# Performance work log

Measured on AMD Instinct MI355X. Metric: run time of the kernel, lower is better.

The kernel has to match this reference:

```python
import jax, jax.numpy as jnp
import numpy as np

D = 1024
H = 16
FF = 4 * D


def layer_norm(x, g, b, eps=1e-5):
    mu = jnp.mean(x, axis=-1, keepdims=True)
    var = jnp.var(x, axis=-1, keepdims=True)
    return (x - mu) * jax.lax.rsqrt(var + eps) * g + b


def setup_inputs() -> dict:
    key = jax.random.key(0)
    ks = jax.random.split(key, 8)
    s = lambda fan_in: 1.0 / np.sqrt(fan_in)
    return {
        "x": jax.random.normal(ks[0], (2, 2048, D), dtype=jnp.float32),
        "ln1_g": jnp.ones((D,), jnp.float32),
        "ln1_b": jnp.zeros((D,), jnp.float32),
        "w_qkv": jax.random.uniform(ks[1], (D, 3 * D), jnp.float32, -s(D), s(D)),
        "b_qkv": jnp.zeros((3 * D,), jnp.float32),
        "w_out": jax.random.uniform(ks[2], (D, D), jnp.float32, -s(D), s(D)),
        "b_out": jnp.zeros((D,), jnp.float32),
        "ln2_g": jnp.ones((D,), jnp.float32),
        "ln2_b": jnp.zeros((D,), jnp.float32),
        "w_fc1": jax.random.uniform(ks[3], (D, FF), jnp.float32, -s(D), s(D)),
        "b_fc1": jnp.zeros((FF,), jnp.float32),
        "w_fc2": jax.random.uniform(ks[4], (FF, D), jnp.float32, -s(FF), s(FF)),
        "b_fc2": jnp.zeros((D,), jnp.float32),
    }


def reference(x, ln1_g, ln1_b, w_qkv, b_qkv, w_out, b_out,
              ln2_g, ln2_b, w_fc1, b_fc1, w_fc2, b_fc2):
    b, n, c = x.shape
    hd = c // H
    scale = hd ** -0.5

    # --- pre-norm MHA ---
    h = layer_norm(x, ln1_g, ln1_b)
    qkv = h @ w_qkv + b_qkv                      # [b,n,3c]
    qkv = qkv.reshape(b, n, 3, H, hd)
    q = jnp.transpose(qkv[:, :, 0], (0, 2, 1, 3))  # [b,H,n,hd]
    k = jnp.transpose(qkv[:, :, 1], (0, 2, 1, 3))
    v = jnp.transpose(qkv[:, :, 2], (0, 2, 1, 3))
    attn = jnp.einsum('bhqd,bhkd->bhqk', q, k) * scale
    attn = jax.nn.softmax(attn, axis=-1)
    o = jnp.einsum('bhqk,bhkd->bhqd', attn, v)   # [b,H,n,hd]
    o = jnp.transpose(o, (0, 2, 1, 3)).reshape(b, n, c)
    x = x + (o @ w_out + b_out)

    # --- pre-norm FFN ---
    h = layer_norm(x, ln2_g, ln2_b)
    h = jax.nn.gelu(h @ w_fc1 + b_fc1, approximate=False)
    x = x + (h @ w_fc2 + b_fc2)
    return x
```

## Files before the change

kernel.cpp:

```cpp
#include <hip/hip_runtime.h>
#include <stdint.h>
#include <math.h>

#define D_MODEL 1024
#define NHEAD   16
#define HDIM    64
#define FFDIM   4096
#define SEQ     2048
#define BATCH   2
#define NTOK    (BATCH*SEQ)
#define QKVN    (3*D_MODEL)

typedef __bf16 bf16;
typedef __attribute__((ext_vector_type(8))) __bf16 bf16x8;
typedef __attribute__((ext_vector_type(4))) __bf16 bf16x4;
typedef __attribute__((ext_vector_type(4))) float f32x4;

__device__ __forceinline__ void gld_lds16(const void* g, void* l) {
    __builtin_amdgcn_global_load_lds((__attribute__((address_space(1))) void*)g,
                                     (__attribute__((address_space(3))) void*)l,
                                     16, 0, 0);
}

__device__ __forceinline__ float fast_exp2(float x) {
#if __has_builtin(__builtin_amdgcn_exp2f)
    return __builtin_amdgcn_exp2f(x);
#else
    return __expf(x * 0.69314718056f);
#endif
}

#define GEMM_BAR() do {                                        \
    asm volatile("s_waitcnt lgkmcnt(0)" ::: "memory");         \
    __builtin_amdgcn_s_barrier();                              \
    asm volatile("" ::: "memory");                             \
} while (0)

__global__ __launch_bounds__(256)
void k_transpose_all(const float* __restrict__ w_qkv, const float* __restrict__ w_out,
                     const float* __restrict__ w_fc1, const float* __restrict__ w_fc2,
                     bf16* __restrict__ t_qkv, bf16* __restrict__ t_out,
                     bf16* __restrict__ t_fc1, bf16* __restrict__ t_fc2) {
    __shared__ float tile[32][33];
    int bid = blockIdx.x;
    const float* W; bf16* Wt; int K, N, ti;
    if (bid < 3072)       { W = w_qkv; Wt = t_qkv; K = 1024; N = 3072; ti = bid; }
    else if (bid < 4096)  { W = w_out; Wt = t_out; K = 1024; N = 1024; ti = bid - 3072; }
    else if (bid < 8192)  { W = w_fc1; Wt = t_fc1; K = 1024; N = 4096; ti = bid - 4096; }
    else                  { W = w_fc2; Wt = t_fc2; K = 4096; N = 1024; ti = bid - 8192; }
    int tn = N >> 5;
    int n0 = (ti % tn) * 32, k0 = (ti / tn) * 32;
    int tx = threadIdx.x, ty = threadIdx.y;
#pragma unroll
    for (int i = 0; i < 4; i++)
        tile[ty + i * 8][tx] = W[(size_t)(k0 + ty + i * 8) * N + n0 + tx];
    __syncthreads();
#pragma unroll
    for (int i = 0; i < 4; i++)
        Wt[(size_t)(n0 + ty + i * 8) * K + k0 + tx] = (bf16)tile[tx][ty + i * 8];
}

__global__ __launch_bounds__(256)
void k_vtrans(const bf16* __restrict__ qkv, bf16* __restrict__ vT) {
    __shared__ bf16 t[32][33];
    int tok0 = blockIdx.x * 32, f0 = blockIdx.y * 32;
    int tx = threadIdx.x, ty = threadIdx.y;
#pragma unroll
    for (int i = 0; i < 4; i++)
        t[ty + i * 8][tx] = qkv[(size_t)(tok0 + ty + i * 8) * QKVN + 2 * D_MODEL + f0 + tx];
    __syncthreads();
    int s = tx;
    int pp = (s < 16) ? ((s >> 2) * 8 + (s & 3))
                      : (((s - 16) >> 2) * 8 + ((s - 16) & 3) + 4);
#pragma unroll
    for (int i = 0; i < 4; i++)
        vT[(size_t)(f0 + ty + i * 8) * NTOK + tok0 + pp] = t[tx][ty + i * 8];
}

__global__ __launch_bounds__(256)
void k_layernorm(const float* __restrict__ x, const float* __restrict__ g,
                 const float* __restrict__ b, bf16* __restrict__ out) {
    int row = blockIdx.x;
    int tid = threadIdx.x;
    float4 v = ((const float4*)(x + (size_t)row * D_MODEL))[tid];
    float s  = v.x + v.y + v.z + v.w;
    float ss = v.x * v.x + v.y * v.y + v.z * v.z + v.w * v.w;
#pragma unroll
    for (int off = 32; off > 0; off >>= 1) {
        s  += __shfl_down(s, off, 64);
        ss += __shfl_down(ss, off, 64);
    }
    __shared__ float red[2][4];
    __shared__ float mv[2];
    int wave = tid >> 6, lane = tid & 63;
    if (lane == 0) { red[0][wave] = s; red[1][wave] = ss; }
    __syncthreads();
    if (tid == 0) {
        float S  = red[0][0] + red[0][1] + red[0][2] + red[0][3];
        float SS = red[1][0] + red[1][1] + red[1][2] + red[1][3];
        float mu = S * (1.0f / D_MODEL);
        float var = SS * (1.0f / D_MODEL) - mu * mu;
        mv[0] = mu;
        mv[1] = rsqrtf(var + 1e-5f);
    }
    __syncthreads();
    float mu = mv[0], rs = mv[1];
    float4 gv = ((const float4*)g)[tid];
    float4 bv = ((const float4*)b)[tid];
    bf16x4 ov = { (bf16)((v.x - mu) * rs * gv.x + bv.x),
                  (bf16)((v.y - mu) * rs * gv.y + bv.y),
                  (bf16)((v.z - mu) * rs * gv.z + bv.z),
                  (bf16)((v.w - mu) * rs * gv.w + bv.w) };
    *(bf16x4*)(out + (size_t)row * D_MODEL + tid * 4) = ov;
}

template <int DO_GELU, int DO_RES, int OUT_BF16, int BN, int PIPE2, int SPLITK>
__global__ __launch_bounds__(256)
void k_gemm(const bf16* __restrict__ A, const bf16* __restrict__ Bt,
            const float* __restrict__ bias, const float* __restrict__ res,
            float* __restrict__ outf, bf16* __restrict__ outb,
            float* __restrict__ part, int M, int N, int K) {
    constexpr int WN = BN / 32;
    __shared__ bf16 As[2][128 * 32];
    __shared__ bf16 Bs[2][BN * 32];
    int tid  = threadIdx.x;
    int wave = tid >> 6, lane = tid & 63;
    int quad = lane >> 4, l16 = lane & 15;

    int nwg = gridDim.x * gridDim.y;
    int bid = blockIdx.y * gridDim.x + blockIdx.x;
    int sid = (bid & 7) * (nwg >> 3) + (bid >> 3);
    int bx = sid % gridDim.x, by = sid / gridDim.x;
    int m0 = by * 128, n0 = bx * BN;
    int wm = (wave >> 1) * 64, wn = (wave & 1) * (BN / 2);

    int Keff = (SPLITK == 2) ? (K >> 1) : K;
    int koff = (SPLITK == 2) ? blockIdx.z * Keff : 0;

    f32x4 acc[4][WN];
#pragma unroll
    for (int i = 0; i < 4; i++)
#pragma unroll
        for (int j = 0; j < WN; j++) acc[i][j] = (f32x4){0.f, 0.f, 0.f, 0.f};

    int lrow = lane >> 2;
    int lcol = (lane & 3) * 8;
    const bf16* gA0 = A + (size_t)(m0 + wave * 32 + lrow) * K + koff + lcol;
    const bf16* gA1 = gA0 + (size_t)16 * K;
    const bf16* gB0;
    const bf16* gB1 = nullptr;
    if constexpr (BN == 128) {
        gB0 = Bt + (size_t)(n0 + wave * 32 + lrow) * K + koff + lcol;
        gB1 = gB0 + (size_t)16 * K;
    } else {
        gB0 = Bt + (size_t)(n0 + wave * 16 + lrow) * K + koff + lcol;
    }

    int wA0 = wave * 1024 + lane * 8;
    int wA1 = wA0 + 512;
    int wB0 = (BN == 128) ? (wave * 1024 + lane * 8) : (wave * 512 + lane * 8);
    int wB1 = wB0 + 512;

    auto issue = [&](bf16x8* r, int k0) {
        r[0] = *(const bf16x8*)(gA0 + k0);
        r[1] = *(const bf16x8*)(gA1 + k0);
        r[2] = *(const bf16x8*)(gB0 + k0);
        if constexpr (BN == 128) r[3] = *(const bf16x8*)(gB1 + k0);
    };
    auto commit = [&](int buf, const bf16x8* r) {
        *(bf16x8*)(&As[buf][wA0]) = r[0];
        *(bf16x8*)(&As[buf][wA1]) = r[1];
        *(bf16x8*)(&Bs[buf][wB0]) = r[2];
        if constexpr (BN == 128) *(bf16x8*)(&Bs[buf][wB1]) = r[3];
    };
    auto compute = [&](int buf) {
        bf16x8 af[4], bfr[WN];
#pragma unroll
        for (int mi = 0; mi < 4; mi++)
            af[mi] = *(const bf16x8*)(&As[buf][(wm + mi * 16 + l16) * 32 + quad * 8]);
#pragma unroll
        for (int ni = 0; ni < WN; ni++)
            bfr[ni] = *(const bf16x8*)(&Bs[buf][(wn + ni * 16 + l16) * 32 + quad * 8]);
#pragma unroll
        for (int mi = 0; mi < 4; mi++)
#pragma unroll
            for (int ni = 0; ni < WN; ni++)
                acc[mi][ni] = __builtin_amdgcn_mfma_f32_16x16x32_bf16(af[mi], bfr[ni], acc[mi][ni], 0, 0, 0);
    };

    int niter = Keff / 32;
    bf16x8 r0[4], r1[4];

    if constexpr (!PIPE2) {
        issue(r0, 0);
        commit(0, r0);
        __syncthreads();
        for (int t = 1; t < niter; t++) {
            issue(r0, t * 32);
            compute((t - 1) & 1);
            commit(t & 1, r0);
            __syncthreads();
        }
        compute((niter - 1) & 1);
    } else {
        issue(r0, 0);
        commit(0, r0);
        issue(r1, 32);
        GEMM_BAR();
        for (int t = 1; t + 2 < niter; t += 2) {
            issue(r0, (t + 1) * 32);
            compute(0);
            commit(1, r1);
            GEMM_BAR();
            issue(r1, (t + 2) * 32);
            compute(1);
            commit(0, r0);
            GEMM_BAR();
        }
        compute(0);
        commit(1, r1);
        GEMM_BAR();
        compute(1);
    }

#pragma unroll
    for (int mi = 0; mi < 4; mi++) {
        int row = m0 + wm + mi * 16 + quad * 4;
#pragma unroll
        for (int ni = 0; ni < WN; ni++) {
            int col = n0 + wn + ni * 16 + l16;
            if constexpr (SPLITK == 2) {
                if (blockIdx.z == 1) {
#pragma unroll
                    for (int r = 0; r < 4; r++)
                        part[(size_t)(row + r) * N + col] = acc[mi][ni][r];
                    continue;
                }
            }
            float bb = bias[col];
#pragma unroll
            for (int r = 0; r < 4; r++) {
                float v = acc[mi][ni][r] + bb;
                if (DO_GELU) v = 0.5f * v * (1.0f + erff(v * 0.70710678118f));
                size_t idx = (size_t)(row + r) * N + col;
                if (DO_RES) v += res[idx];
                if (OUT_BF16) outb[idx] = (bf16)v;
                else          outf[idx] = v;
            }
        }
    }
}

__global__ __launch_bounds__(256)
void k_add(float* __restrict__ out, const float* __restrict__ part) {
    size_t i = (size_t)blockIdx.x * 256 + threadIdx.x;
    float4* o = (float4*)out;
    const float4* p = (const float4*)part;
    float4 a = o[i], q = p[i];
    a.x += q.x; a.y += q.y; a.z += q.z; a.w += q.w;
    o[i] = a;
}

__global__ __launch_bounds__(256)
void k_attention2(const bf16* __restrict__ qkv, const bf16* __restrict__ vT,
                  bf16* __restrict__ o) {
    __shared__ bf16 Ks[2][64][32];
    __shared__ bf16 Vs[2][64][32];

    int tid = threadIdx.x, wave = tid >> 6, lane = tid & 63;
    int quad = lane >> 4, l16 = lane & 15;
    int bh = blockIdx.y;
    int b = bh >> 4, h = bh & 15;
    int q0 = blockIdx.x * 64 + wave * 16;

    const bf16* Qb  = qkv + (size_t)b * SEQ * QKVN + h * HDIM;
    const bf16* Kb  = Qb + D_MODEL;
    const bf16* vTb = vT + (size_t)h * HDIM * NTOK + b * SEQ;

    const float QSCALE = 0.125f * 1.44269504089f;
    bf16x8 qf[2];
#pragma unroll
    for (int c = 0; c < 2; c++) {
        bf16x8 qraw = *(const bf16x8*)(Qb + (size_t)(q0 + l16) * QKVN + c * 32 + quad * 8);
#pragma unroll
        for (int i = 0; i < 8; i++) qf[c][i] = (bf16)((float)qraw[i] * QSCALE);
    }

    const bf16* gK0 = Kb + (size_t)(wave * 16 + (lane >> 2)) * QKVN + 0 * 32 + (lane & 3) * 8;
    const bf16* gK1 = gK0 + 32;
    const bf16* gV0 = vTb + (size_t)(wave * 16 + (lane >> 2)) * NTOK + (lane & 3) * 8;
    const bf16* gV1 = gV0 + 32;
    bf16* lK0 = &Ks[0][wave * 16][0];
    bf16* lK1 = &Ks[1][wave * 16][0];
    bf16* lV0 = &Vs[0][wave * 16][0];
    bf16* lV1 = &Vs[1][wave * 16][0];

    f32x4 oacc[4];
#pragma unroll
    for (int i = 0; i < 4; i++) oacc[i] = (f32x4){0.f, 0.f, 0.f, 0.f};
    float lsum = 0.f;

    for (int kv0 = 0; kv0 < SEQ; kv0 += 64) {
        __syncthreads();
        size_t koff = (size_t)kv0 * QKVN;
        gld_lds16(gK0 + koff, lK0);
        gld_lds16(gK1 + koff, lK1);
        gld_lds16(gV0 + kv0, lV0);
        gld_lds16(gV1 + kv0, lV1);
        __syncthreads();

        f32x4 s[4];
#pragma unroll
        for (int t = 0; t < 4; t++) {
            bf16x8 af0 = *(const bf16x8*)(&Ks[0][t * 16 + l16][quad * 8]);
            bf16x8 af1 = *(const bf16x8*)(&Ks[1][t * 16 + l16][quad * 8]);
            f32x4 z = (f32x4){0.f, 0.f, 0.f, 0.f};
            z = __builtin_amdgcn_mfma_f32_16x16x32_bf16(af0, qf[0], z, 0, 0, 0);
            z = __builtin_amdgcn_mfma_f32_16x16x32_bf16(af1, qf[1], z, 0, 0, 0);
            s[t] = z;
        }

        bf16x4 p[4];
#pragma unroll
        for (int t = 0; t < 4; t++)
#pragma unroll
            for (int r = 0; r < 4; r++) {
                float pf = fast_exp2(s[t][r]);
                lsum += pf;
                p[t][r] = (bf16)pf;
            }

#pragma unroll
        for (int tp = 0; tp < 2; tp++) {
            bf16x8 pa = __builtin_shufflevector(p[2 * tp], p[2 * tp + 1], 0, 1, 2, 3, 4, 5, 6, 7);
#pragma unroll
            for (int nt = 0; nt < 4; nt++) {
                bf16x8 vb = *(const bf16x8*)(&Vs[tp][nt * 16 + l16][quad * 8]);
                oacc[nt] = __builtin_amdgcn_mfma_f32_16x16x32_bf16(pa, vb, oacc[nt], 0, 0, 0);
            }
        }
    }

    lsum += __shfl_xor(lsum, 16, 64);
    lsum += __shfl_xor(lsum, 32, 64);
    float invl[4];
#pragma unroll
    for (int r = 0; r < 4; r++)
        invl[r] = 1.0f / __shfl(lsum, quad * 4 + r, 16);

#pragma unroll
    for (int nt = 0; nt < 4; nt++)
#pragma unroll
        for (int r = 0; r < 4; r++)
            o[(size_t)(b * SEQ + q0 + quad * 4 + r) * D_MODEL + h * HDIM + nt * 16 + l16] =
                (bf16)(oacc[nt][r] * invl[r]);
}

extern "C" void kernel_launch(void* const* d_in, const int* in_sizes, int n_in,
                              void* d_out, int out_size, void* d_ws, size_t ws_size,
                              hipStream_t stream) {
    const float* x     = (const float*)d_in[0];
    const float* ln1_g = (const float*)d_in[1];
    const float* ln1_b = (const float*)d_in[2];
    const float* w_qkv = (const float*)d_in[3];
    const float* b_qkv = (const float*)d_in[4];
    const float* w_out = (const float*)d_in[5];
    const float* b_out = (const float*)d_in[6];
    const float* ln2_g = (const float*)d_in[7];
    const float* ln2_b = (const float*)d_in[8];
    const float* w_fc1 = (const float*)d_in[9];
    const float* b_fc1 = (const float*)d_in[10];
    const float* w_fc2 = (const float*)d_in[11];
    const float* b_fc2 = (const float*)d_in[12];
    float* out = (float*)d_out;

    uintptr_t ws = (uintptr_t)d_ws;
    bf16* wt_qkv = (bf16*)(ws + 0);
    bf16* wt_out = (bf16*)(ws + 6291456);
    bf16* wt_fc1 = (bf16*)(ws + 8388608);
    bf16* wt_fc2 = (bf16*)(ws + 16777216);
    bf16* hbuf   = (bf16*)(ws + 25165824);
    bf16* vT     = hbuf;
    bf16* qkv    = (bf16*)(ws + 33554432);
    bf16* attn_o = (bf16*)(ws + 58720256);
    bf16* hgelu  = (bf16*)(ws + 33554432);
    float* fc2p  = (float*)(ws + 0);

    k_transpose_all<<<12288, dim3(32, 8), 0, stream>>>(w_qkv, w_out, w_fc1, w_fc2,
                                                       wt_qkv, wt_out, wt_fc1, wt_fc2);

    k_layernorm<<<NTOK, 256, 0, stream>>>(x, ln1_g, ln1_b, hbuf);

    k_gemm<0, 0, 1, 128, 0, 1><<<dim3(QKVN / 128, NTOK / 128), 256, 0, stream>>>(
        hbuf, wt_qkv, b_qkv, nullptr, nullptr, qkv, nullptr, NTOK, QKVN, D_MODEL);

    k_vtrans<<<dim3(NTOK / 32, D_MODEL / 32), dim3(32, 8), 0, stream>>>(qkv, vT);

    k_attention2<<<dim3(SEQ / 64, BATCH * NHEAD), 256, 0, stream>>>(qkv, vT, attn_o);

    k_gemm<0, 1, 0, 64, 1, 1><<<dim3(D_MODEL / 64, NTOK / 128), 256, 0, stream>>>(
        attn_o, wt_out, b_out, x, out, nullptr, nullptr, NTOK, D_MODEL, D_MODEL);

    k_layernorm<<<NTOK, 256, 0, stream>>>(out, ln2_g, ln2_b, hbuf);

    k_gemm<1, 0, 1, 128, 0, 1><<<dim3(FFDIM / 128, NTOK / 128), 256, 0, stream>>>(
        hbuf, wt_fc1, b_fc1, nullptr, nullptr, hgelu, nullptr, NTOK, FFDIM, D_MODEL);

    k_gemm<0, 1, 0, 128, 1, 2><<<dim3(D_MODEL / 128, NTOK / 128, 2), 256, 0, stream>>>(
        hgelu, wt_fc2, b_fc2, out, out, nullptr, fc2p, NTOK, D_MODEL, FFDIM);

    k_add<<<(NTOK * D_MODEL / 4) / 256, 256, 0, stream>>>(out, fc2p);
}
```

Measured before the change: 367.6 us.

## Use direct global-to-LDS single-buffer loads in QKV/FC1 GEMMs and fast tanh GELU

Adds a STAGE template path that loads A/B tiles straight into LDS with global_load_lds, using one buffer and two barriers per K step. The QKV and FC1 GEMMs switch to this path to skip the register staging and halve LDS use, which may allow more resident workgroups. The price is no overlap between loading and MFMA compute within a workgroup. Separately, exact erf GELU is replaced by a tanh approximation built from exp2 and rcp, which changes numerics slightly.

```diff
diff --git a/kernel.cpp b/kernel.cpp
--- a/kernel.cpp
+++ b/kernel.cpp
@@ -28,6 +28,22 @@
 #else
     return __expf(x * 0.69314718056f);
 #endif
+}
+
+__device__ __forceinline__ float fast_rcp(float x) {
+#if __has_builtin(__builtin_amdgcn_rcpf)
+    return __builtin_amdgcn_rcpf(x);
+#else
+    return 1.0f / x;
+#endif
+}
+
+__device__ __forceinline__ float gelu_fast(float x) {
+    float xx = x * x;
+    float y  = x * fmaf(0.035677408137f, xx, 0.7978845608f);
+    float z  = fminf(-2.8853900817779268f * y, 126.0f);
+    float e  = fast_exp2(z);
+    return x * fast_rcp(1.0f + e);
 }
 
 #define GEMM_BAR() do {                                        \
@@ -114,15 +130,16 @@
     *(bf16x4*)(out + (size_t)row * D_MODEL + tid * 4) = ov;
 }
 
-template <int DO_GELU, int DO_RES, int OUT_BF16, int BN, int PIPE2, int SPLITK>
+template <int DO_GELU, int DO_RES, int OUT_BF16, int BN, int PIPE2, int SPLITK, int STAGE>
 __global__ __launch_bounds__(256)
 void k_gemm(const bf16* __restrict__ A, const bf16* __restrict__ Bt,
             const float* __restrict__ bias, const float* __restrict__ res,
             float* __restrict__ outf, bf16* __restrict__ outb,
             float* __restrict__ part, int M, int N, int K) {
     constexpr int WN = BN / 32;
-    __shared__ bf16 As[2][128 * 32];
-    __shared__ bf16 Bs[2][BN * 32];
+    constexpr int NBUF = STAGE ? 1 : 2;
+    __shared__ bf16 As[NBUF][128 * 32];
+    __shared__ bf16 Bs[NBUF][BN * 32];
     int tid  = threadIdx.x;
     int wave = tid >> 6, lane = tid & 63;
     int quad = lane >> 4, l16 = lane & 15;
@@ -189,9 +206,24 @@
     };
 
     int niter = Keff / 32;
-    bf16x8 r0[4], r1[4];
-
-    if constexpr (!PIPE2) {
+
+    if constexpr (STAGE == 1) {
+        bf16* lA0 = &As[0][wave * 1024];
+        bf16* lA1 = lA0 + 512;
+        bf16* lB0 = &Bs[0][(BN == 128) ? wave * 1024 : wave * 512];
+        bf16* lB1 = lB0 + 512;
+        for (int t = 0; t < niter; t++) {
+            int k0 = t * 32;
+            __syncthreads();
+            gld_lds16(gA0 + k0, lA0);
+            gld_lds16(gA1 + k0, lA1);
+            gld_lds16(gB0 + k0, lB0);
+            if constexpr (BN == 128) gld_lds16(gB1 + k0, lB1);
+            __syncthreads();
+            compute(0);
+        }
+    } else if constexpr (!PIPE2) {
+        bf16x8 r0[4];
         issue(r0, 0);
         commit(0, r0);
         __syncthreads();
@@ -203,6 +235,7 @@
         }
         compute((niter - 1) & 1);
     } else {
+        bf16x8 r0[4], r1[4];
         issue(r0, 0);
         commit(0, r0);
         issue(r1, 32);
@@ -241,7 +274,7 @@
 #pragma unroll
             for (int r = 0; r < 4; r++) {
                 float v = acc[mi][ni][r] + bb;
-                if (DO_GELU) v = 0.5f * v * (1.0f + erff(v * 0.70710678118f));
+                if (DO_GELU) v = gelu_fast(v);
                 size_t idx = (size_t)(row + r) * N + col;
                 if (DO_RES) v += res[idx];
                 if (OUT_BF16) outb[idx] = (bf16)v;
@@ -391,22 +424,22 @@
 
     k_layernorm<<<NTOK, 256, 0, stream>>>(x, ln1_g, ln1_b, hbuf);
 
-    k_gemm<0, 0, 1, 128, 0, 1><<<dim3(QKVN / 128, NTOK / 128), 256, 0, stream>>>(
+    k_gemm<0, 0, 1, 128, 0, 1, 1><<<dim3(QKVN / 128, NTOK / 128), 256, 0, stream>>>(
         hbuf, wt_qkv, b_qkv, nullptr, nullptr, qkv, nullptr, NTOK, QKVN, D_MODEL);
 
     k_vtrans<<<dim3(NTOK / 32, D_MODEL / 32), dim3(32, 8), 0, stream>>>(qkv, vT);
 
     k_attention2<<<dim3(SEQ / 64, BATCH * NHEAD), 256, 0, stream>>>(qkv, vT, attn_o);
 
-    k_gemm<0, 1, 0, 64, 1, 1><<<dim3(D_MODEL / 64, NTOK / 128), 256, 0, stream>>>(
+    k_gemm<0, 1, 0, 64, 1, 1, 0><<<dim3(D_MODEL / 64, NTOK / 128), 256, 0, stream>>>(
         attn_o, wt_out, b_out, x, out, nullptr, nullptr, NTOK, D_MODEL, D_MODEL);
 
     k_layernorm<<<NTOK, 256, 0, stream>>>(out, ln2_g, ln2_b, hbuf);
 
-    k_gemm<1, 0, 1, 128, 0, 1><<<dim3(FFDIM / 128, NTOK / 128), 256, 0, stream>>>(
+    k_gemm<1, 0, 1, 128, 0, 1, 1><<<dim3(FFDIM / 128, NTOK / 128), 256, 0, stream>>>(
         hbuf, wt_fc1, b_fc1, nullptr, nullptr, hgelu, nullptr, NTOK, FFDIM, D_MODEL);
 
-    k_gemm<0, 1, 0, 128, 1, 2><<<dim3(D_MODEL / 128, NTOK / 128, 2), 256, 0, stream>>>(
+    k_gemm<0, 1, 0, 128, 1, 2, 0><<<dim3(D_MODEL / 128, NTOK / 128, 2), 256, 0, stream>>>(
         hgelu, wt_fc2, b_fc2, out, out, nullptr, fc2p, NTOK, D_MODEL, FFDIM);
 
     k_add<<<(NTOK * D_MODEL / 4) / 256, 256, 0, stream>>>(out, fc2p);
```

Result: no change. 365.3 us (-0.6%).
